# Kernel tuning notes

Measured on AMD Instinct MI355X. Metric: run time of the kernel, lower is better.

The kernel has to match this reference:

```python
import jax, jax.numpy as jnp
import numpy as np

N_NODES = 100000
N_EDGES = 3200000
N_GRAPHS = 128


def setup_inputs() -> dict:
    key = jax.random.key(0)
    ks = jax.random.split(key, 16)
    x = jax.random.normal(ks[0], (N_NODES, 47), dtype=jnp.float32)
    edge_index = jax.random.randint(ks[1], (2, N_EDGES), 0, N_NODES, dtype=jnp.int32)
    batch = jnp.sort(jax.random.randint(ks[2], (N_NODES,), 0, N_GRAPHS, dtype=jnp.int32))

    def w(k, shape):
        fan_in = shape[0]
        return jax.random.normal(k, shape, dtype=jnp.float32) * (1.0 / np.sqrt(fan_in))

    return {
        "x": x, "edge_index": edge_index, "batch": batch,
        "W1": w(ks[3], (47, 64)), "b1": jnp.zeros((64,), jnp.float32),
        "W2": w(ks[4], (64, 32)), "b2": jnp.zeros((32,), jnp.float32),
        "A1": w(ks[5], (32, 32)), "c1": jnp.zeros((32,), jnp.float32),
        "A2": w(ks[6], (32, 16)), "c2": jnp.zeros((16,), jnp.float32),
        "A3": w(ks[7], (16, 8)),  "c3": jnp.zeros((8,), jnp.float32),
        "A4": w(ks[8], (8, 1)),   "c4": jnp.zeros((1,), jnp.float32),
    }


def _gcn_conv(x, W, b, src, dst):
    # PyG GCNConv: h = XW, then D^-1/2 (A+I) D^-1/2 aggregation, then + bias.
    h = x @ W  # [N, out]
    ones = jnp.ones(dst.shape[0], dtype=h.dtype)
    deg = jax.ops.segment_sum(ones, dst, num_segments=N_NODES)  # incl. self loops
    dinv = jnp.where(deg > 0, jax.lax.rsqrt(deg), 0.0)
    norm = dinv[src] * dinv[dst]  # [E_total]
    msg = h[src] * norm[:, None]  # gather + normalize
    out = jax.ops.segment_sum(msg, dst, num_segments=N_NODES)  # scatter-add
    return out + b


def reference(x, edge_index, batch, W1, b1, W2, b2, A1, c1, A2, c2, A3, c3, A4, c4):
    loops = jnp.arange(N_NODES, dtype=edge_index.dtype)
    src = jnp.concatenate([edge_index[0], loops])
    dst = jnp.concatenate([edge_index[1], loops])
    h = jax.nn.relu(_gcn_conv(x, W1, b1, src, dst))
    h = jax.nn.relu(_gcn_conv(h, W2, b2, src, dst))
    # dropout is identity in eval mode
    g = jax.ops.segment_sum(h, batch, num_segments=N_GRAPHS)  # global_add_pool [G,32]
    g = jax.nn.relu(g @ A1 + c1)
    g = jax.nn.relu(g @ A2 + c2)
    g = jax.nn.relu(g @ A3 + c3)
    return g @ A4 + c4  # [G, 1]
```

## Files before the change

kernel.cpp:

```cpp
#include <hip/hip_runtime.h>

#define N_NODES 100000
#define N_EDGES 3200000
#define N_GRAPHS 128

#define RSHIFT 8
#define NPR 256
#define R_RANGES ((N_NODES + NPR - 1) / NPR)
#define CAP 9472
#define C_CHUNKS 512
#define EPC (N_EDGES / C_CHUNKS)
#define SRC_BITS 17

#define XPB 64
#define AXW 48

__device__ inline unsigned short f2bf(float f) {
    unsigned u = __float_as_uint(f);
    unsigned r = u + 0x7FFFu + ((u >> 16) & 1u);
    return (unsigned short)(r >> 16);
}
__device__ inline float bflo(unsigned u) { return __uint_as_float(u << 16); }
__device__ inline float bfhi(unsigned u) { return __uint_as_float(u & 0xFFFF0000u); }


__global__ __launch_bounds__(256) void padcvt_kernel(const float* __restrict__ x,
                                                     unsigned short* __restrict__ xpb,
                                                     int* __restrict__ range_next) {
    if (blockIdx.x < 2) {
        int i = blockIdx.x * 256 + threadIdx.x;
        if (i < R_RANGES) range_next[i] = i * CAP;
    }
    int idx = blockIdx.x * 256 + threadIdx.x;
    if (idx >= N_NODES * XPB) return;
    int n = idx >> 6;
    int c = idx & 63;
    float v = (c < 47) ? x[n * 47 + c] : 0.f;
    xpb[idx] = f2bf(v);
}


__global__ __launch_bounds__(256) void partition_kernel(const int* __restrict__ src,
                                                        const int* __restrict__ dst,
                                                        int* __restrict__ range_next,
                                                        int* __restrict__ bucket) {
    __shared__ int cntL[R_RANGES];
    __shared__ int baseL[R_RANGES];
    const int t = threadIdx.x, b = blockIdx.x;
    const int e0 = b * EPC, e1 = e0 + EPC;
    for (int i = t; i < R_RANGES; i += 256) cntL[i] = 0;
    __syncthreads();
    for (int e = e0 + t; e < e1; e += 256) atomicAdd(&cntL[dst[e] >> RSHIFT], 1);
    __syncthreads();
    for (int i = t; i < R_RANGES; i += 256) {
        int c = cntL[i];
        baseL[i] = (c > 0) ? atomicAdd(&range_next[i], c) : 0;
        cntL[i] = 0;
    }
    __syncthreads();
    for (int e = e0 + t; e < e1; e += 256) {
        int d = dst[e];
        int s = src[e];
        int r = d >> RSHIFT;
        int p = baseL[r] + atomicAdd(&cntL[r], 1);
        if (p < (r + 1) * CAP)
            bucket[p] = ((d & (NPR - 1)) << SRC_BITS) | s;
    }
}


__global__ __launch_bounds__(256) void build_kernel(const int* __restrict__ bucket,
                                                    const int* __restrict__ range_next,
                                                    int* __restrict__ row_ptr,
                                                    int* __restrict__ row_cnt,
                                                    float* __restrict__ dinv,
                                                    int* __restrict__ csr_src) {
    __shared__ int sE[CAP];
    __shared__ int degs[NPR];
    __shared__ int part[256];
    const int t = threadIdx.x, r = blockIdx.x;
    const int base_node = r * NPR;
    const int seg0 = r * CAP;
    int m = range_next[r] - seg0;
    if (m > CAP) m = CAP;
    for (int i = t; i < m; i += 256) sE[i] = bucket[seg0 + i];
    degs[t] = 0;
    __syncthreads();
    for (int i = t; i < m; i += 256) atomicAdd(&degs[sE[i] >> SRC_BITS], 1);
    __syncthreads();
    int d = degs[t];
    part[t] = d;
    __syncthreads();
    for (int dd = 1; dd < 256; dd <<= 1) {
        int tv = (t >= dd) ? part[t - dd] : 0;
        __syncthreads();
        part[t] += tv;
        __syncthreads();
    }
    int ex = part[t] - d;
    int node = base_node + t;
    if (node < N_NODES) {
        row_ptr[node] = seg0 + ex;
        row_cnt[node] = d;
        dinv[node] = rsqrtf((float)(d + 1));
    }
    degs[t] = ex;
    __syncthreads();
    for (int i = t; i < m; i += 256) {
        int p = sE[i];
        int pos = atomicAdd(&degs[p >> SRC_BITS], 1);
        csr_src[seg0 + pos] = p & ((1 << SRC_BITS) - 1);
    }
}


__global__ __launch_bounds__(256) void aggXZ_kernel(const unsigned short* __restrict__ xpb,
                                                    const float* __restrict__ dinv,
                                                    const int* __restrict__ row_ptr,
                                                    const int* __restrict__ row_cnt,
                                                    const int* __restrict__ csr_src,
                                                    const float* __restrict__ W1,
                                                    const float* __restrict__ b1,
                                                    const float* __restrict__ W2,
                                                    unsigned short* __restrict__ zb) {
    __shared__ float W1s[AXW * 64];
    __shared__ float W2s[64 * 32];
    __shared__ float b1s[64];
    __shared__ float rows[4][AXW];
    __shared__ float ts[4][64];
    const int t = threadIdx.x;
    for (int i = t; i < 47 * 64; i += 256) W1s[i] = W1[i];
    for (int i = t; i < 64; i += 256) { W1s[47 * 64 + i] = 0.f; b1s[i] = b1[i]; }
    for (int i = t; i < 64 * 32; i += 256) W2s[i] = W2[i];

    const int nn = t >> 6;
    const int n = blockIdx.x * 4 + nn;
    const int l = t & 63;
    const int eo = l >> 3;
    const int cg = l & 7;
    const float dn = dinv[n];

    float acc[8] = {0.f, 0.f, 0.f, 0.f, 0.f, 0.f, 0.f, 0.f};
    {
        if (eo == 0) {
            uint4 q = *(const uint4*)(xpb + (size_t)n * XPB + cg * 8);
            float w = dn * dn;
            acc[0] = bflo(q.x) * w; acc[1] = bfhi(q.x) * w;
            acc[2] = bflo(q.y) * w; acc[3] = bfhi(q.y) * w;
            acc[4] = bflo(q.z) * w; acc[5] = bfhi(q.z) * w;
            acc[6] = bflo(q.w) * w; acc[7] = bfhi(q.w) * w;
        }
    }
    const int st = row_ptr[n];
    const int cnt = row_cnt[n];
    int k = eo;
    for (; k + 8 < cnt; k += 16) {
        int s0 = csr_src[st + k];
        int s1 = csr_src[st + k + 8];
        float w0 = dinv[s0] * dn;
        float w1 = dinv[s1] * dn;
        uint4 q0 = *(const uint4*)(xpb + (size_t)s0 * XPB + cg * 8);
        uint4 q1 = *(const uint4*)(xpb + (size_t)s1 * XPB + cg * 8);
        acc[0] = fmaf(bflo(q0.x), w0, acc[0]); acc[1] = fmaf(bfhi(q0.x), w0, acc[1]);
        acc[2] = fmaf(bflo(q0.y), w0, acc[2]); acc[3] = fmaf(bfhi(q0.y), w0, acc[3]);
        acc[4] = fmaf(bflo(q0.z), w0, acc[4]); acc[5] = fmaf(bfhi(q0.z), w0, acc[5]);
        acc[6] = fmaf(bflo(q0.w), w0, acc[6]); acc[7] = fmaf(bfhi(q0.w), w0, acc[7]);
        acc[0] = fmaf(bflo(q1.x), w1, acc[0]); acc[1] = fmaf(bfhi(q1.x), w1, acc[1]);
        acc[2] = fmaf(bflo(q1.y), w1, acc[2]); acc[3] = fmaf(bfhi(q1.y), w1, acc[3]);
        acc[4] = fmaf(bflo(q1.z), w1, acc[4]); acc[5] = fmaf(bfhi(q1.z), w1, acc[5]);
        acc[6] = fmaf(bflo(q1.w), w1, acc[6]); acc[7] = fmaf(bfhi(q1.w), w1, acc[7]);
    }
    if (k < cnt) {
        int s0 = csr_src[st + k];
        float w0 = dinv[s0] * dn;
        uint4 q0 = *(const uint4*)(xpb + (size_t)s0 * XPB + cg * 8);
        acc[0] = fmaf(bflo(q0.x), w0, acc[0]); acc[1] = fmaf(bfhi(q0.x), w0, acc[1]);
        acc[2] = fmaf(bflo(q0.y), w0, acc[2]); acc[3] = fmaf(bfhi(q0.y), w0, acc[3]);
        acc[4] = fmaf(bflo(q0.z), w0, acc[4]); acc[5] = fmaf(bfhi(q0.z), w0, acc[5]);
        acc[6] = fmaf(bflo(q0.w), w0, acc[6]); acc[7] = fmaf(bfhi(q0.w), w0, acc[7]);
    }
#pragma unroll
    for (int off = 8; off <= 32; off <<= 1) {
#pragma unroll
        for (int j = 0; j < 8; ++j) acc[j] += __shfl_xor(acc[j], off);
    }
    if (eo == 0 && cg < 6) {
#pragma unroll
        for (int j = 0; j < 8; ++j) rows[nn][cg * 8 + j] = acc[j];
    }
    __syncthreads();
    {
        const int c = t & 63;
        float s = b1s[c];
#pragma unroll
        for (int kk = 0; kk < AXW; ++kk) s = fmaf(rows[nn][kk], W1s[kk * 64 + c], s);
        ts[nn][c] = fmaxf(s, 0.f);
    }
    __syncthreads();
    if (t < 128) {
        const int n2 = t >> 5, c = t & 31;
        float s = 0.f;
#pragma unroll
        for (int kk = 0; kk < 64; ++kk) s = fmaf(ts[n2][kk], W2s[kk * 32 + c], s);
        zb[(size_t)(blockIdx.x * 4 + n2) * 32 + c] = f2bf(s);
    }
}


__global__ __launch_bounds__(256) void aggregate32_kernel(const unsigned short* __restrict__ zb,
                                                          const float* __restrict__ dinv,
                                                          const int* __restrict__ row_ptr,
                                                          const int* __restrict__ row_cnt,
                                                          const int* __restrict__ csr_src,
                                                          const float* __restrict__ bias,
                                                          float* __restrict__ out) {
    const int tid = threadIdx.x;
    const int n = blockIdx.x * 4 + (tid >> 6);
    if (n >= N_NODES) return;
    const int l = tid & 63;
    const int eo = l >> 2;
    const int cg = l & 3;
    const float dn = dinv[n];

    float acc[8] = {0.f, 0.f, 0.f, 0.f, 0.f, 0.f, 0.f, 0.f};
    if (eo == 0) {
        uint4 q = *(const uint4*)(zb + (size_t)n * 32 + cg * 8);
        float w = dn * dn;
        acc[0] = bflo(q.x) * w; acc[1] = bfhi(q.x) * w;
        acc[2] = bflo(q.y) * w; acc[3] = bfhi(q.y) * w;
        acc[4] = bflo(q.z) * w; acc[5] = bfhi(q.z) * w;
        acc[6] = bflo(q.w) * w; acc[7] = bfhi(q.w) * w;
    }
    const int st = row_ptr[n];
    const int cnt = row_cnt[n];
    int k = eo;
    for (; k + 16 < cnt; k += 32) {
        int s0 = csr_src[st + k];
        int s1 = csr_src[st + k + 16];
        float w0 = dinv[s0] * dn;
        float w1 = dinv[s1] * dn;
        uint4 q0 = *(const uint4*)(zb + (size_t)s0 * 32 + cg * 8);
        uint4 q1 = *(const uint4*)(zb + (size_t)s1 * 32 + cg * 8);
        acc[0] = fmaf(bflo(q0.x), w0, acc[0]); acc[1] = fmaf(bfhi(q0.x), w0, acc[1]);
        acc[2] = fmaf(bflo(q0.y), w0, acc[2]); acc[3] = fmaf(bfhi(q0.y), w0, acc[3]);
        acc[4] = fmaf(bflo(q0.z), w0, acc[4]); acc[5] = fmaf(bfhi(q0.z), w0, acc[5]);
        acc[6] = fmaf(bflo(q0.w), w0, acc[6]); acc[7] = fmaf(bfhi(q0.w), w0, acc[7]);
        acc[0] = fmaf(bflo(q1.x), w1, acc[0]); acc[1] = fmaf(bfhi(q1.x), w1, acc[1]);
        acc[2] = fmaf(bflo(q1.y), w1, acc[2]); acc[3] = fmaf(bfhi(q1.y), w1, acc[3]);
        acc[4] = fmaf(bflo(q1.z), w1, acc[4]); acc[5] = fmaf(bfhi(q1.z), w1, acc[5]);
        acc[6] = fmaf(bflo(q1.w), w1, acc[6]); acc[7] = fmaf(bfhi(q1.w), w1, acc[7]);
    }
    if (k < cnt) {
        int s0 = csr_src[st + k];
        float w0 = dinv[s0] * dn;
        uint4 q0 = *(const uint4*)(zb + (size_t)s0 * 32 + cg * 8);
        acc[0] = fmaf(bflo(q0.x), w0, acc[0]); acc[1] = fmaf(bfhi(q0.x), w0, acc[1]);
        acc[2] = fmaf(bflo(q0.y), w0, acc[2]); acc[3] = fmaf(bfhi(q0.y), w0, acc[3]);
        acc[4] = fmaf(bflo(q0.z), w0, acc[4]); acc[5] = fmaf(bfhi(q0.z), w0, acc[5]);
        acc[6] = fmaf(bflo(q0.w), w0, acc[6]); acc[7] = fmaf(bfhi(q0.w), w0, acc[7]);
    }
#pragma unroll
    for (int off = 4; off <= 32; off <<= 1) {
#pragma unroll
        for (int j = 0; j < 8; ++j) acc[j] += __shfl_xor(acc[j], off);
    }
    if (eo == 0) {
        const float* bp = bias + cg * 8;
        float4 a, b;
        a.x = fmaxf(acc[0] + bp[0], 0.f);
        a.y = fmaxf(acc[1] + bp[1], 0.f);
        a.z = fmaxf(acc[2] + bp[2], 0.f);
        a.w = fmaxf(acc[3] + bp[3], 0.f);
        b.x = fmaxf(acc[4] + bp[4], 0.f);
        b.y = fmaxf(acc[5] + bp[5], 0.f);
        b.z = fmaxf(acc[6] + bp[6], 0.f);
        b.w = fmaxf(acc[7] + bp[7], 0.f);
        *(float4*)(out + (size_t)n * 32 + cg * 8) = a;
        *(float4*)(out + (size_t)n * 32 + cg * 8 + 4) = b;
    }
}


#define POOL_NPB 256

__global__ __launch_bounds__(256) void pool_kernel(const int* __restrict__ batch,
                                                   const float* __restrict__ h,
                                                   float* __restrict__ g) {
    const int t = threadIdx.x;
    const int c = t & 31;
    const int r = t >> 5;
    int i0 = blockIdx.x * POOL_NPB;
    int i1 = i0 + POOL_NPB;
    if (i1 > N_NODES) i1 = N_NODES;
    int cur_g = -1;
    float acc = 0.f;
    for (int i = i0 + r; i < i1; i += 8) {
        int gi = batch[i];
        float v = h[(size_t)i * 32 + c];
        if (gi != cur_g) {
            if (cur_g >= 0) atomicAdd(&g[cur_g * 32 + c], acc);
            acc = 0.f;
            cur_g = gi;
        }
        acc += v;
    }
    if (cur_g >= 0) atomicAdd(&g[cur_g * 32 + c], acc);
}


__global__ __launch_bounds__(128) void mlp_kernel(const float* __restrict__ g,
                                                  const float* __restrict__ A1, const float* __restrict__ c1,
                                                  const float* __restrict__ A2, const float* __restrict__ c2,
                                                  const float* __restrict__ A3, const float* __restrict__ c3,
                                                  const float* __restrict__ A4, const float* __restrict__ c4,
                                                  float* __restrict__ out) {
    int t = threadIdx.x;
    float v[32];
#pragma unroll
    for (int k = 0; k < 32; ++k) v[k] = g[t * 32 + k];
    float u[32];
#pragma unroll
    for (int c = 0; c < 32; ++c) {
        float s = c1[c];
#pragma unroll
        for (int k = 0; k < 32; ++k) s = fmaf(v[k], A1[k * 32 + c], s);
        u[c] = fmaxf(s, 0.f);
    }
    float w[16];
#pragma unroll
    for (int c = 0; c < 16; ++c) {
        float s = c2[c];
#pragma unroll
        for (int k = 0; k < 32; ++k) s = fmaf(u[k], A2[k * 16 + c], s);
        w[c] = fmaxf(s, 0.f);
    }
    float z[8];
#pragma unroll
    for (int c = 0; c < 8; ++c) {
        float s = c3[c];
#pragma unroll
        for (int k = 0; k < 16; ++k) s = fmaf(w[k], A3[k * 8 + c], s);
        z[c] = fmaxf(s, 0.f);
    }
    float s = c4[0];
#pragma unroll
    for (int k = 0; k < 8; ++k) s = fmaf(z[k], A4[k], s);
    out[t] = s;
}


extern "C" void kernel_launch(void* const* d_in, const int* in_sizes, int n_in,
                              void* d_out, int out_size, void* d_ws, size_t ws_size,
                              hipStream_t stream) {
    const float* x    = (const float*)d_in[0];
    const int*   ei   = (const int*)d_in[1];
    const int*   srcE = ei;
    const int*   dstE = ei + N_EDGES;
    const int*   batch = (const int*)d_in[2];
    const float* W1 = (const float*)d_in[3];  const float* b1 = (const float*)d_in[4];
    const float* W2 = (const float*)d_in[5];  const float* b2 = (const float*)d_in[6];
    const float* A1 = (const float*)d_in[7];  const float* c1 = (const float*)d_in[8];
    const float* A2 = (const float*)d_in[9];  const float* c2 = (const float*)d_in[10];
    const float* A3 = (const float*)d_in[11]; const float* c3 = (const float*)d_in[12];
    const float* A4 = (const float*)d_in[13]; const float* c4 = (const float*)d_in[14];
    float* out = (float*)d_out;

    char* ws = (char*)d_ws;
    size_t off_b = 0;
    auto take = [&](size_t bytes) -> char* {
        char* p = ws + off_b;
        off_b = (off_b + bytes + 255) & ~(size_t)255;
        return p;
    };
    int*            row_ptr    = (int*)take((size_t)N_NODES * 4);
    int*            row_cnt    = (int*)take((size_t)N_NODES * 4);
    float*          dinv       = (float*)take((size_t)N_NODES * 4);
    int*            range_next = (int*)take((size_t)R_RANGES * 4);
    int*            csr_src    = (int*)take((size_t)R_RANGES * CAP * 4);
    char*           bz_raw     = take((size_t)R_RANGES * CAP * 4);
    int*            bucket     = (int*)bz_raw;
    unsigned short* zb         = (unsigned short*)bz_raw;
    unsigned short* xpb        = (unsigned short*)take((size_t)N_NODES * XPB * 2);
    float*          agg        = (float*)take((size_t)N_NODES * 32 * 4);
    float*          g          = (float*)take((size_t)N_GRAPHS * 32 * 4);
    (void)ws_size; (void)in_sizes; (void)n_in; (void)out_size;

    padcvt_kernel<<<(N_NODES * XPB + 255) / 256, 256, 0, stream>>>(x, xpb, range_next);

    partition_kernel<<<C_CHUNKS, 256, 0, stream>>>(srcE, dstE, range_next, bucket);
    build_kernel<<<R_RANGES, 256, 0, stream>>>(bucket, range_next, row_ptr, row_cnt, dinv, csr_src);

    aggXZ_kernel<<<N_NODES / 4, 256, 0, stream>>>(xpb, dinv, row_ptr, row_cnt, csr_src,
                                                  W1, b1, W2, zb);
    aggregate32_kernel<<<(N_NODES + 3) / 4, 256, 0, stream>>>(zb, dinv, row_ptr, row_cnt, csr_src, b2, agg);

    hipMemsetAsync(g, 0, (size_t)N_GRAPHS * 32 * 4, stream);
    pool_kernel<<<(N_NODES + POOL_NPB - 1) / POOL_NPB, 256, 0, stream>>>(batch, agg, g);
    mlp_kernel<<<1, 128, 0, stream>>>(g, A1, c1, A2, c2, A3, c3, A4, c4, out);
}
```

Before: 406.3 us.

## Precompute per-edge source weights and split aggregation from dense GEMMs

A new kernel writes a per-edge array holding dinv[src] in CSR order, so both aggregation kernels read the weight contiguously instead of doing a random gather of dinv per edge. The fused layer-1 kernel is also split in two. One kernel only aggregates and writes bf16 rows. A second kernel loads W1 and W2 into shared memory once per 100 nodes and applies both GEMMs, instead of reloading the weights for every 4 nodes. This adds a kernel launch, an extra edge-sized array, and a round trip of the aggregated features through global memory.

```diff
diff --git a/kernel.cpp b/kernel.cpp
--- a/kernel.cpp
+++ b/kernel.cpp
@@ -114,42 +114,43 @@
 }
 
 
-__global__ __launch_bounds__(256) void aggXZ_kernel(const unsigned short* __restrict__ xpb,
+__global__ __launch_bounds__(256) void wprep_kernel(const int* __restrict__ csr_src,
+                                                    const int* __restrict__ range_next,
                                                     const float* __restrict__ dinv,
-                                                    const int* __restrict__ row_ptr,
-                                                    const int* __restrict__ row_cnt,
-                                                    const int* __restrict__ csr_src,
-                                                    const float* __restrict__ W1,
-                                                    const float* __restrict__ b1,
-                                                    const float* __restrict__ W2,
-                                                    unsigned short* __restrict__ zb) {
-    __shared__ float W1s[AXW * 64];
-    __shared__ float W2s[64 * 32];
-    __shared__ float b1s[64];
-    __shared__ float rows[4][AXW];
-    __shared__ float ts[4][64];
-    const int t = threadIdx.x;
-    for (int i = t; i < 47 * 64; i += 256) W1s[i] = W1[i];
-    for (int i = t; i < 64; i += 256) { W1s[47 * 64 + i] = 0.f; b1s[i] = b1[i]; }
-    for (int i = t; i < 64 * 32; i += 256) W2s[i] = W2[i];
-
-    const int nn = t >> 6;
-    const int n = blockIdx.x * 4 + nn;
-    const int l = t & 63;
+                                                    float* __restrict__ csr_w) {
+    const int t = threadIdx.x, r = blockIdx.x;
+    const int seg0 = r * CAP;
+    int m = range_next[r] - seg0;
+    if (m > CAP) m = CAP;
+    for (int i = t; i < m; i += 256) {
+        csr_w[seg0 + i] = dinv[csr_src[seg0 + i]];
+    }
+}
+
+
+__global__ __launch_bounds__(256) void aggX_kernel(const unsigned short* __restrict__ xpb,
+                                                   const float* __restrict__ dinv,
+                                                   const int* __restrict__ row_ptr,
+                                                   const int* __restrict__ row_cnt,
+                                                   const int* __restrict__ csr_src,
+                                                   const float* __restrict__ csr_w,
+                                                   unsigned short* __restrict__ aggxb) {
+    const int tid = threadIdx.x;
+    const int n = blockIdx.x * 4 + (tid >> 6);
+    if (n >= N_NODES) return;
+    const int l = tid & 63;
     const int eo = l >> 3;
     const int cg = l & 7;
     const float dn = dinv[n];
 
     float acc[8] = {0.f, 0.f, 0.f, 0.f, 0.f, 0.f, 0.f, 0.f};
-    {
-        if (eo == 0) {
-            uint4 q = *(const uint4*)(xpb + (size_t)n * XPB + cg * 8);
-            float w = dn * dn;
-            acc[0] = bflo(q.x) * w; acc[1] = bfhi(q.x) * w;
-            acc[2] = bflo(q.y) * w; acc[3] = bfhi(q.y) * w;
-            acc[4] = bflo(q.z) * w; acc[5] = bfhi(q.z) * w;
-            acc[6] = bflo(q.w) * w; acc[7] = bfhi(q.w) * w;
-        }
+    if (eo == 0) {
+        uint4 q = *(const uint4*)(xpb + (size_t)n * XPB + cg * 8);
+        float w = dn * dn;
+        acc[0] = bflo(q.x) * w; acc[1] = bfhi(q.x) * w;
+        acc[2] = bflo(q.y) * w; acc[3] = bfhi(q.y) * w;
+        acc[4] = bflo(q.z) * w; acc[5] = bfhi(q.z) * w;
+        acc[6] = bflo(q.w) * w; acc[7] = bfhi(q.w) * w;
     }
     const int st = row_ptr[n];
     const int cnt = row_cnt[n];
@@ -157,8 +158,8 @@
     for (; k + 8 < cnt; k += 16) {
         int s0 = csr_src[st + k];
         int s1 = csr_src[st + k + 8];
-        float w0 = dinv[s0] * dn;
-        float w1 = dinv[s1] * dn;
+        float w0 = csr_w[st + k] * dn;
+        float w1 = csr_w[st + k + 8] * dn;
         uint4 q0 = *(const uint4*)(xpb + (size_t)s0 * XPB + cg * 8);
         uint4 q1 = *(const uint4*)(xpb + (size_t)s1 * XPB + cg * 8);
         acc[0] = fmaf(bflo(q0.x), w0, acc[0]); acc[1] = fmaf(bfhi(q0.x), w0, acc[1]);
@@ -172,7 +173,7 @@
     }
     if (k < cnt) {
         int s0 = csr_src[st + k];
-        float w0 = dinv[s0] * dn;
+        float w0 = csr_w[st + k] * dn;
         uint4 q0 = *(const uint4*)(xpb + (size_t)s0 * XPB + cg * 8);
         acc[0] = fmaf(bflo(q0.x), w0, acc[0]); acc[1] = fmaf(bfhi(q0.x), w0, acc[1]);
         acc[2] = fmaf(bflo(q0.y), w0, acc[2]); acc[3] = fmaf(bfhi(q0.y), w0, acc[3]);
@@ -185,24 +186,57 @@
         for (int j = 0; j < 8; ++j) acc[j] += __shfl_xor(acc[j], off);
     }
     if (eo == 0 && cg < 6) {
-#pragma unroll
-        for (int j = 0; j < 8; ++j) rows[nn][cg * 8 + j] = acc[j];
-    }
-    __syncthreads();
-    {
-        const int c = t & 63;
-        float s = b1s[c];
-#pragma unroll
-        for (int kk = 0; kk < AXW; ++kk) s = fmaf(rows[nn][kk], W1s[kk * 64 + c], s);
-        ts[nn][c] = fmaxf(s, 0.f);
-    }
-    __syncthreads();
-    if (t < 128) {
-        const int n2 = t >> 5, c = t & 31;
-        float s = 0.f;
-#pragma unroll
-        for (int kk = 0; kk < 64; ++kk) s = fmaf(ts[n2][kk], W2s[kk * 32 + c], s);
-        zb[(size_t)(blockIdx.x * 4 + n2) * 32 + c] = f2bf(s);
+        uint4 o;
+        o.x = ((unsigned)f2bf(acc[1]) << 16) | f2bf(acc[0]);
+        o.y = ((unsigned)f2bf(acc[3]) << 16) | f2bf(acc[2]);
+        o.z = ((unsigned)f2bf(acc[5]) << 16) | f2bf(acc[4]);
+        o.w = ((unsigned)f2bf(acc[7]) << 16) | f2bf(acc[6]);
+        *(uint4*)(aggxb + (size_t)n * AXW + cg * 8) = o;
+    }
+}
+
+
+#define GB_NODES 100
+
+__global__ __launch_bounds__(256) void fusedgemm_kernel(const unsigned short* __restrict__ aggxb,
+                                                        const float* __restrict__ W1,
+                                                        const float* __restrict__ b1,
+                                                        const float* __restrict__ W2,
+                                                        unsigned short* __restrict__ zb) {
+    __shared__ float W1s[AXW * 64];
+    __shared__ float W2s[64 * 32];
+    __shared__ float b1s[64];
+    __shared__ float rows[4][AXW];
+    __shared__ float ts[4][64];
+    const int t = threadIdx.x;
+    for (int i = t; i < 47 * 64; i += 256) W1s[i] = W1[i];
+    for (int i = t; i < 64; i += 256) { W1s[47 * 64 + i] = 0.f; b1s[i] = b1[i]; }
+    for (int i = t; i < 64 * 32; i += 256) W2s[i] = W2[i];
+    __syncthreads();
+
+    const int base = blockIdx.x * GB_NODES;
+    for (int pass = 0; pass < GB_NODES / 4; ++pass) {
+        const int nb = base + pass * 4;
+        if (t < 4 * AXW) {
+            rows[t / AXW][t % AXW] = bflo(aggxb[(size_t)nb * AXW + t]);
+        }
+        __syncthreads();
+        {
+            const int nn = t >> 6, c = t & 63;
+            float s = b1s[c];
+#pragma unroll
+            for (int k = 0; k < AXW; ++k) s = fmaf(rows[nn][k], W1s[k * 64 + c], s);
+            ts[nn][c] = fmaxf(s, 0.f);
+        }
+        __syncthreads();
+        if (t < 128) {
+            const int nn = t >> 5, c = t & 31;
+            float s = 0.f;
+#pragma unroll
+            for (int k = 0; k < 64; ++k) s = fmaf(ts[nn][k], W2s[k * 32 + c], s);
+            zb[(size_t)(nb + nn) * 32 + c] = f2bf(s);
+        }
+        __syncthreads();
     }
 }
 
@@ -212,6 +246,7 @@
                                                           const int* __restrict__ row_ptr,
                                                           const int* __restrict__ row_cnt,
                                                           const int* __restrict__ csr_src,
+                                                          const float* __restrict__ csr_w,
                                                           const float* __restrict__ bias,
                                                           float* __restrict__ out) {
     const int tid = threadIdx.x;
@@ -237,8 +272,8 @@
     for (; k + 16 < cnt; k += 32) {
         int s0 = csr_src[st + k];
         int s1 = csr_src[st + k + 16];
-        float w0 = dinv[s0] * dn;
-        float w1 = dinv[s1] * dn;
+        float w0 = csr_w[st + k] * dn;
+        float w1 = csr_w[st + k + 16] * dn;
         uint4 q0 = *(const uint4*)(zb + (size_t)s0 * 32 + cg * 8);
         uint4 q1 = *(const uint4*)(zb + (size_t)s1 * 32 + cg * 8);
         acc[0] = fmaf(bflo(q0.x), w0, acc[0]); acc[1] = fmaf(bfhi(q0.x), w0, acc[1]);
@@ -252,7 +287,7 @@
     }
     if (k < cnt) {
         int s0 = csr_src[st + k];
-        float w0 = dinv[s0] * dn;
+        float w0 = csr_w[st + k] * dn;
         uint4 q0 = *(const uint4*)(zb + (size_t)s0 * 32 + cg * 8);
         acc[0] = fmaf(bflo(q0.x), w0, acc[0]); acc[1] = fmaf(bfhi(q0.x), w0, acc[1]);
         acc[2] = fmaf(bflo(q0.y), w0, acc[2]); acc[3] = fmaf(bfhi(q0.y), w0, acc[3]);
@@ -377,11 +412,14 @@
     float*          dinv       = (float*)take((size_t)N_NODES * 4);
     int*            range_next = (int*)take((size_t)R_RANGES * 4);
     int*            csr_src    = (int*)take((size_t)R_RANGES * CAP * 4);
+    float*          csr_w      = (float*)take((size_t)R_RANGES * CAP * 4);
     char*           bz_raw     = take((size_t)R_RANGES * CAP * 4);
     int*            bucket     = (int*)bz_raw;
     unsigned short* zb         = (unsigned short*)bz_raw;
     unsigned short* xpb        = (unsigned short*)take((size_t)N_NODES * XPB * 2);
-    float*          agg        = (float*)take((size_t)N_NODES * 32 * 4);
+    char*           aa_raw     = take((size_t)N_NODES * 32 * 4);
+    unsigned short* aggxb      = (unsigned short*)aa_raw;
+    float*          agg        = (float*)aa_raw;
     float*          g          = (float*)take((size_t)N_GRAPHS * 32 * 4);
     (void)ws_size; (void)in_sizes; (void)n_in; (void)out_size;
 
@@ -389,10 +427,11 @@
 
     partition_kernel<<<C_CHUNKS, 256, 0, stream>>>(srcE, dstE, range_next, bucket);
     build_kernel<<<R_RANGES, 256, 0, stream>>>(bucket, range_next, row_ptr, row_cnt, dinv, csr_src);
-
-    aggXZ_kernel<<<N_NODES / 4, 256, 0, stream>>>(xpb, dinv, row_ptr, row_cnt, csr_src,
-                                                  W1, b1, W2, zb);
-    aggregate32_kernel<<<(N_NODES + 3) / 4, 256, 0, stream>>>(zb, dinv, row_ptr, row_cnt, csr_src, b2, agg);
+    wprep_kernel<<<R_RANGES, 256, 0, stream>>>(csr_src, range_next, dinv, csr_w);
+
+    aggX_kernel<<<(N_NODES + 3) / 4, 256, 0, stream>>>(xpb, dinv, row_ptr, row_cnt, csr_src, csr_w, aggxb);
+    fusedgemm_kernel<<<N_NODES / GB_NODES, 256, 0, stream>>>(aggxb, W1, b1, W2, zb);
+    aggregate32_kernel<<<(N_NODES + 3) / 4, 256, 0, stream>>>(zb, dinv, row_ptr, row_cnt, csr_src, csr_w, b2, agg);
 
     hipMemsetAsync(g, 0, (size_t)N_GRAPHS * 32 * 4, stream);
     pool_kernel<<<(N_NODES + POOL_NPB - 1) / POOL_NPB, 256, 0, stream>>>(batch, agg, g);
```

Measured after the change: 390.3 us. -3.9%, faster.
